# Performance work log

Hardware: AMD Instinct MI355X
Metric: run time of the kernel (lower is better)

Reference implementation:

```python
import jax, jax.numpy as jnp
import numpy as np

LN_EPS = 1e-5

def setup_inputs() -> dict:
    key = jax.random.key(0)
    ks = jax.random.split(key, 16)
    B, N, D, H = 8, 256, 128, 128
    s = 0.02
    inp = {
        'h': jax.random.normal(ks[0], (B, N, D), jnp.float32),
        'x': jax.random.normal(ks[1], (B, N, 3), jnp.float32),
        'mask': jax.random.randint(ks[2], (B, N), 0, 2, jnp.int32),
        # edge_mlp: Linear(2D+1,H), SiLU, Linear(H,H), SiLU
        'we1': jax.random.normal(ks[3], (2 * D + 1, H), jnp.float32) * s,
        'be1': jnp.zeros((H,), jnp.float32),
        'we2': jax.random.normal(ks[4], (H, H), jnp.float32) * s,
        'be2': jnp.zeros((H,), jnp.float32),
        # node_mlp: Linear(H+D,H), SiLU, Linear(H,D)
        'wn1': jax.random.normal(ks[5], (H + D, H), jnp.float32) * s,
        'bn1': jnp.zeros((H,), jnp.float32),
        'wn2': jax.random.normal(ks[6], (H, D), jnp.float32) * s,
        'bn2': jnp.zeros((D,), jnp.float32),
        # coord_mlp: Linear(H,H), SiLU, Linear(H,1,bias=False) xavier gain 1e-3, Tanh
        'wc1': jax.random.normal(ks[7], (H, H), jnp.float32) * s,
        'bc1': jnp.zeros((H,), jnp.float32),
        'wc2': jax.random.normal(ks[8], (H, 1), jnp.float32) * 0.001,
        # layer norm over output_nf
        'gamma': jnp.ones((D,), jnp.float32),
        'beta': jnp.zeros((D,), jnp.float32),
    }
    return inp


def reference(h, x, mask, we1, be1, we2, be2, wn1, bn1, wn2, bn2, wc1, bc1, wc2, gamma, beta):
    B, N, D = h.shape
    m = mask.astype(h.dtype)                      # [B,N]
    cm = m[:, :, None] * m[:, None, :]            # [B,N,N]

    hi = jnp.broadcast_to(h[:, :, None, :], (B, N, N, D))
    hj = jnp.broadcast_to(h[:, None, :, :], (B, N, N, D))
    rel_x = x[:, :, None, :] - x[:, None, :, :]   # [B,N,N,3]
    dist_sq = jnp.sum(rel_x * rel_x, axis=-1, keepdims=True) + 1e-8

    edge_input = jnp.concatenate([hi, hj, dist_sq], axis=-1)  # [B,N,N,2D+1]
    m_ij = jax.nn.silu(jax.nn.silu(edge_input @ we1 + be1) @ we2 + be2)
    m_ij = m_ij * cm[..., None]                   # [B,N,N,H]

    w_ij = jnp.tanh(jax.nn.silu(m_ij @ wc1 + bc1) @ wc2) * 0.1
    w_ij = w_ij * cm[..., None]                   # [B,N,N,1]

    coord_diff = jnp.sum(rel_x * w_ij, axis=2) / N
    x_out = x + coord_diff

    agg_m = jnp.sum(m_ij, axis=2)                 # [B,N,H]
    h_new = jax.nn.silu(jnp.concatenate([h, agg_m], axis=-1) @ wn1 + bn1) @ wn2 + bn2
    h2 = h + h_new

    mu = jnp.mean(h2, axis=-1, keepdims=True)
    var = jnp.mean((h2 - mu) ** 2, axis=-1, keepdims=True)
    h_out = (h2 - mu) * jax.lax.rsqrt(var + LN_EPS) * gamma + beta
    return (h_out, x_out)
```

## Files before the change

### kernel.cpp

```cpp
#include <hip/hip_runtime.h>
#include <hip/hip_bf16.h>

using short8 = __attribute__((ext_vector_type(8))) short;
using f32x4  = __attribute__((ext_vector_type(4))) float;

#define HD 128
#define NN 256
#define NB 2048

static __device__ __forceinline__ unsigned short us(float v) {
    union { __hip_bfloat16 b; unsigned short s; } c; c.b = __float2bfloat16(v); return c.s;
}
static __device__ __forceinline__ unsigned int pk2(float a, float b) {
    return (unsigned int)us(a) | ((unsigned int)us(b) << 16);
}
static __device__ __forceinline__ float fsilu(float v) {
    return __fdividef(v, 1.f + __expf(-v));
}
static __device__ __forceinline__ float ftanh(float v) {
    return 1.f - __fdividef(2.f, __expf(2.f * v) + 1.f);
}
static __device__ __forceinline__ int swz(int row, int kbyte) { return row * 256 + (kbyte ^ ((row & 7) << 4)); }
static __device__ __forceinline__ int swz512(int row, int kbyte) { return row * 512 + (kbyte ^ ((row & 7) << 4)); }

__global__ __launch_bounds__(256) void prep_all(
    const float* __restrict__ we2, const float* __restrict__ wc1,
    const float* __restrict__ wn1, const float* __restrict__ wn2,
    const float* __restrict__ we1, const int* __restrict__ mask,
    unsigned short* __restrict__ we2pk, unsigned short* __restrict__ wc1pk,
    unsigned short* __restrict__ wn1pk, unsigned short* __restrict__ wn2pk,
    unsigned short* __restrict__ we1pk,
    int* __restrict__ idxB, int* __restrict__ cntB)
{
    const int blk = blockIdx.x;
    const int t = threadIdx.x;
    if (blk < 448) {
        const int idx = blk * 256 + t;
        if (idx < 81920) {
            const float* src; unsigned short* dst; int local;
            if (idx < 16384)      { src = we2; dst = we2pk; local = idx;         }
            else if (idx < 32768) { src = wc1; dst = wc1pk; local = idx - 16384; }
            else if (idx < 65536) { src = wn1; dst = wn1pk; local = idx - 32768; }
            else                  { src = wn2; dst = wn2pk; local = idx - 65536; }
            const int k = local >> 7, n = local & 127;
            dst[((k >> 3) * 128 + n) * 8 + (k & 7)] = us(src[local]);
        } else {
            const int local = idx - 81920;
            const int k = local >> 8, n = local & 255;
            const int srci = (n < HD) ? (k * HD + n) : ((HD + k) * HD + (n - HD));
            we1pk[((k >> 3) * 256 + n) * 8 + (k & 7)] = us(we1[srci]);
        }
    } else {
        const int b = blk - 448;
        const int lane = t & 63, wvp = t >> 6;
        const int m = mask[b * NN + t];
        const unsigned long long bal = __ballot(m != 0);
        const int pos = __popcll(bal & ((1ULL << lane) - 1ULL));
        __shared__ int wc[4];
        if (lane == 0) wc[wvp] = __popcll(bal);
        __syncthreads();
        int base = 0;
        for (int w = 0; w < wvp; ++w) base += wc[w];
        const int cnt = wc[0] + wc[1] + wc[2] + wc[3];
        const int act_before = base + pos;
        const int slot = m ? act_before : cnt + (t - act_before);
        idxB[b * NN + slot] = t;
        if (t == 0) cntB[b] = cnt;
    }
}

__global__ __launch_bounds__(256) void prep_node_mfma(
    const float* __restrict__ h, const unsigned short* __restrict__ we1pk,
    const float* __restrict__ be1,
    float* __restrict__ Apre, float* __restrict__ Bpre)
{
    const int r0 = blockIdx.x * 16;
    const int tid = threadIdx.x;
    const int wv = tid >> 6, lane = tid & 63, g = lane >> 4, cl = lane & 15;
    __shared__ __align__(16) unsigned short t1[16 * HD];
    {
        const int row = tid >> 4, k0 = (tid & 15) * 8;
        const float4 a0 = *(const float4*)(h + (size_t)(r0 + row) * HD + k0);
        const float4 a1 = *(const float4*)(h + (size_t)(r0 + row) * HD + k0 + 4);
        uint4 o;
        o.x = pk2(a0.x, a0.y); o.y = pk2(a0.z, a0.w);
        o.z = pk2(a1.x, a1.y); o.w = pk2(a1.z, a1.w);
        *(uint4*)((char*)t1 + swz(row, 2 * k0)) = o;
    }
    __syncthreads();
    const f32x4 zero4 = {0.f, 0.f, 0.f, 0.f};
    f32x4 acc[4] = {zero4, zero4, zero4, zero4};
    #pragma unroll
    for (int ks = 0; ks < 4; ++ks) {
        const short8 a = *(const short8*)((char*)t1 + swz(cl, ks * 64 + g * 16));
        #pragma unroll
        for (int nt = 0; nt < 4; ++nt) {
            const int col = wv * 64 + nt * 16 + cl;
            const short8 bb = *(const short8*)(we1pk + ((ks * 4 + g) * 256 + col) * 8);
            acc[nt] = __builtin_amdgcn_mfma_f32_16x16x32_bf16(a, bb, acc[nt], 0, 0, 0);
        }
    }
    #pragma unroll
    for (int nt = 0; nt < 4; ++nt) {
        const int col = wv * 64 + nt * 16 + cl;
        const float bias = (col < HD) ? be1[col] : 0.f;
        #pragma unroll
        for (int r = 0; r < 4; ++r) {
            const int row = r0 + g * 4 + r;
            const float v = acc[nt][r] + bias;
            if (col < HD) Apre[(size_t)row * HD + col] = v;
            else          Bpre[(size_t)row * HD + (col - HD)] = v;
        }
    }
}

__global__ __launch_bounds__(256, 3) void egcl_main(
    const float* __restrict__ x, const float* __restrict__ we1,
    const float* __restrict__ be2, const float* __restrict__ bc1,
    const float* __restrict__ wc2,
    const float* __restrict__ Apre, const float* __restrict__ Bpre,
    const unsigned short* __restrict__ we2pk, const unsigned short* __restrict__ wc1pk,
    const int* __restrict__ idxB, const int* __restrict__ cntB,
    float* __restrict__ aggp, float4* __restrict__ cdws)
{
    const int blk = blockIdx.x;
    const int b = blk >> 9;
    const int q = blk & 511;
    const int p = q >> 1, hh = q & 1;
    const int tid = threadIdx.x;
    const int wv = tid >> 6, lane = tid & 63, g = lane >> 4, cl = lane & 15;

    const int cnt = cntB[b];
    const int i = idxB[b * NN + p];
    const int rowb = b * NN + i;

    const int nch_t = (cnt + 15) >> 4;
    const int c0 = ((nch_t + 1) >> 1) << 4;
    const int jbase = hh ? c0 : 0;
    const int jend  = hh ? cnt : (c0 < cnt ? c0 : cnt);
    const int hcnt  = jend - jbase;

    if (p >= cnt || hcnt <= 0) {
        if (tid < HD) aggp[((size_t)hh * NB + rowb) * HD + tid] = 0.f;
        if (tid == 0) cdws[hh * NB + rowb] = make_float4(0.f, 0.f, 0.f, 0.f);
        return;
    }

    __shared__ __align__(16) unsigned short m1[16 * HD];
    __shared__ __align__(16) unsigned short t2[16 * HD];
    __shared__ __align__(16) float4 jx_s[128];
    __shared__ int j_s[128];
    __shared__ __align__(16) float Ai_s[HD], wl_s[HD];
    __shared__ float sws[4][16];
    __shared__ float cdp[4][3];

    const float xi0 = x[rowb * 3 + 0];
    const float xi1 = x[rowb * 3 + 1];
    const float xi2 = x[rowb * 3 + 2];
    const int nch = (hcnt + 15) >> 4;

    if (tid < nch * 16) {
        const int j = (tid < hcnt) ? idxB[b * NN + jbase + tid] : i;
        const float* xj = x + (b * NN + j) * 3;
        const float x0 = xj[0], x1 = xj[1], x2 = xj[2];
        const float dx = xi0 - x0, dy = xi1 - x1, dz = xi2 - x2;
        float4 v; v.x = dx * dx + dy * dy + dz * dz + 1e-8f;
        v.y = x0; v.z = x1; v.w = x2;
        jx_s[tid] = v; j_s[tid] = j;
    }
    if (tid < HD) Ai_s[tid] = Apre[(size_t)rowb * HD + tid];
    else if (tid < 2 * HD) wl_s[tid - HD] = we1[2 * HD * HD + (tid - HD)];

    short8 bw2[4][2], bwc[4][2];
    #pragma unroll
    for (int ks = 0; ks < 4; ++ks) {
        #pragma unroll
        for (int nt = 0; nt < 2; ++nt) {
            const int off = ((ks * 4 + g) * HD + wv * 32 + nt * 16 + cl) * 8;
            bw2[ks][nt] = *(const short8*)(we2pk + off);
            bwc[ks][nt] = *(const short8*)(wc1pk + off);
        }
    }
    float be2v[2], bc1v[2], wc2v[2];
    #pragma unroll
    for (int nt = 0; nt < 2; ++nt) {
        const int col = wv * 32 + nt * 16 + cl;
        be2v[nt] = be2[col]; bc1v[nt] = bc1[col]; wc2v[nt] = wc2[col];
    }

    float agg[2] = {0.f, 0.f};
    float cdx = 0.f, cdy = 0.f, cdz = 0.f;
    const f32x4 zero4 = {0.f, 0.f, 0.f, 0.f};

    const int arow = tid >> 4;
    const int ak0  = (tid & 15) * 8;
    float4 sb0, sb1;

    #define ISSUE(C) do { \
        const float* bp_ = Bpre + (size_t)(b * NN + j_s[(C) * 16 + arow]) * HD + ak0; \
        sb0 = *(const float4*)(bp_); \
        sb1 = *(const float4*)(bp_ + 4); \
    } while (0)

    #define APHASE(C) do { \
        const float d2_ = jx_s[(C) * 16 + arow].x; \
        const float4 a0 = *(const float4*)(Ai_s + ak0); \
        const float4 a1 = *(const float4*)(Ai_s + ak0 + 4); \
        const float4 w0 = *(const float4*)(wl_s + ak0); \
        const float4 w1 = *(const float4*)(wl_s + ak0 + 4); \
        uint4 o; \
        o.x = pk2(fsilu(a0.x + sb0.x + d2_ * w0.x), fsilu(a0.y + sb0.y + d2_ * w0.y)); \
        o.y = pk2(fsilu(a0.z + sb0.z + d2_ * w0.z), fsilu(a0.w + sb0.w + d2_ * w0.w)); \
        o.z = pk2(fsilu(a1.x + sb1.x + d2_ * w1.x), fsilu(a1.y + sb1.y + d2_ * w1.y)); \
        o.w = pk2(fsilu(a1.z + sb1.z + d2_ * w1.z), fsilu(a1.w + sb1.w + d2_ * w1.w)); \
        *(uint4*)((char*)m1 + swz(arow, 2 * ak0)) = o; \
    } while (0)

    __syncthreads();
    ISSUE(0);
    APHASE(0);
    __syncthreads();

    for (int c = 0; c < nch; ++c) {
        f32x4 acc[2] = {zero4, zero4};
        #pragma unroll
        for (int ks = 0; ks < 4; ++ks) {
            const short8 a = *(const short8*)((char*)m1 + swz(cl, 2 * (ks * 32 + g * 8)));
            acc[0] = __builtin_amdgcn_mfma_f32_16x16x32_bf16(a, bw2[ks][0], acc[0], 0, 0, 0);
            acc[1] = __builtin_amdgcn_mfma_f32_16x16x32_bf16(a, bw2[ks][1], acc[1], 0, 0, 0);
        }
        #pragma unroll
        for (int nt = 0; nt < 2; ++nt) {
            const int col = wv * 32 + nt * 16 + cl;
            #pragma unroll
            for (int r = 0; r < 4; ++r) {
                const int row = g * 4 + r;
                const float mp = (c * 16 + row < hcnt) ? 1.f : 0.f;
                const float v = fsilu(acc[nt][r] + be2v[nt]) * mp;
                agg[nt] += v;
                *(unsigned short*)((char*)t2 + swz(row, 2 * col)) = us(v);
            }
        }
        __syncthreads();
        if (c + 1 < nch) ISSUE(c + 1);
        f32x4 acc2[2] = {zero4, zero4};
        #pragma unroll
        for (int ks = 0; ks < 4; ++ks) {
            const short8 a2 = *(const short8*)((char*)t2 + swz(cl, 2 * (ks * 32 + g * 8)));
            acc2[0] = __builtin_amdgcn_mfma_f32_16x16x32_bf16(a2, bwc[ks][0], acc2[0], 0, 0, 0);
            acc2[1] = __builtin_amdgcn_mfma_f32_16x16x32_bf16(a2, bwc[ks][1], acc2[1], 0, 0, 0);
        }
        #pragma unroll
        for (int r = 0; r < 4; ++r) {
            float sr = fsilu(acc2[0][r] + bc1v[0]) * wc2v[0]
                     + fsilu(acc2[1][r] + bc1v[1]) * wc2v[1];
            sr += __shfl_xor(sr, 1); sr += __shfl_xor(sr, 2);
            sr += __shfl_xor(sr, 4); sr += __shfl_xor(sr, 8);
            if (cl == 0) sws[wv][g * 4 + r] = sr;
        }
        if (c + 1 < nch) APHASE(c + 1);
        __syncthreads();
        if (tid < 16 && c * 16 + tid < hcnt) {
            const float s = sws[0][tid] + sws[1][tid] + sws[2][tid] + sws[3][tid];
            const float w = ftanh(s) * 0.1f;
            const float4 jx = jx_s[c * 16 + tid];
            cdx += (xi0 - jx.y) * w;
            cdy += (xi1 - jx.z) * w;
            cdz += (xi2 - jx.w) * w;
        }
    }
    #undef ISSUE
    #undef APHASE

    #pragma unroll
    for (int nt = 0; nt < 2; ++nt) {
        agg[nt] += __shfl_xor(agg[nt], 16);
        agg[nt] += __shfl_xor(agg[nt], 32);
    }
    if (lane < 16) {
        aggp[((size_t)hh * NB + rowb) * HD + wv * 32 + lane]      = agg[0];
        aggp[((size_t)hh * NB + rowb) * HD + wv * 32 + 16 + lane] = agg[1];
    }
    if (tid < 16) {
        cdx += __shfl_xor(cdx, 1); cdx += __shfl_xor(cdx, 2);
        cdx += __shfl_xor(cdx, 4); cdx += __shfl_xor(cdx, 8);
        cdy += __shfl_xor(cdy, 1); cdy += __shfl_xor(cdy, 2);
        cdy += __shfl_xor(cdy, 4); cdy += __shfl_xor(cdy, 8);
        cdz += __shfl_xor(cdz, 1); cdz += __shfl_xor(cdz, 2);
        cdz += __shfl_xor(cdz, 4); cdz += __shfl_xor(cdz, 8);
        if (tid == 0) {
            cdws[hh * NB + rowb] = make_float4(cdx, cdy, cdz, 0.f);
        }
    }
}

__global__ __launch_bounds__(256) void node_mlp(
    const float* __restrict__ h, const float* __restrict__ x,
    const float* __restrict__ aggp, const float4* __restrict__ cdws,
    const unsigned short* __restrict__ wn1pk, const unsigned short* __restrict__ wn2pk,
    const float* __restrict__ bn1, const float* __restrict__ bn2,
    const float* __restrict__ gamma, const float* __restrict__ beta,
    float* __restrict__ hout, float* __restrict__ xout)
{
    const int r0 = blockIdx.x * 16;
    const int tid = threadIdx.x;
    const int wv = tid >> 6, lane = tid & 63, g = lane >> 4, cl = lane & 15;
    __shared__ __align__(16) unsigned short t1[16 * 256];
    __shared__ __align__(16) unsigned short t2[16 * HD];
    __shared__ float rs1[4][16], rs2[4][16];
    __shared__ float bn1_s[HD], bn2_s[HD], gam_s[HD], bet_s[HD];
    if (tid < HD) {
        bn1_s[tid] = bn1[tid]; bn2_s[tid] = bn2[tid];
        gam_s[tid] = gamma[tid]; bet_s[tid] = beta[tid];
    }
    if (tid >= 128 && tid < 144) {
        const int row = r0 + (tid - 128);
        const float4 c0 = cdws[row], c1 = cdws[NB + row];
        xout[row * 3 + 0] = x[row * 3 + 0] + (c0.x + c1.x) * (1.f / 256.f);
        xout[row * 3 + 1] = x[row * 3 + 1] + (c0.y + c1.y) * (1.f / 256.f);
        xout[row * 3 + 2] = x[row * 3 + 2] + (c0.z + c1.z) * (1.f / 256.f);
    }
    {
        const int row = tid >> 4, k0 = (tid & 15) * 16;
        const size_t off = (size_t)(r0 + row) * HD;
        char* dst = (char*)t1;
        if (k0 < HD) {
            #pragma unroll
            for (int u = 0; u < 16; u += 8) {
                const float4 a0 = *(const float4*)(h + off + k0 + u);
                const float4 a1 = *(const float4*)(h + off + k0 + u + 4);
                uint4 o;
                o.x = pk2(a0.x, a0.y); o.y = pk2(a0.z, a0.w);
                o.z = pk2(a1.x, a1.y); o.w = pk2(a1.z, a1.w);
                *(uint4*)(dst + swz512(row, 2 * (k0 + u))) = o;
            }
        } else {
            const int kk = k0 - HD;
            #pragma unroll
            for (int u = 0; u < 16; u += 8) {
                const float4 a0 = *(const float4*)(aggp + off + kk + u);
                const float4 a1 = *(const float4*)(aggp + off + kk + u + 4);
                const float4 b0 = *(const float4*)(aggp + (size_t)NB * HD + off + kk + u);
                const float4 b1 = *(const float4*)(aggp + (size_t)NB * HD + off + kk + u + 4);
                uint4 o;
                o.x = pk2(a0.x + b0.x, a0.y + b0.y); o.y = pk2(a0.z + b0.z, a0.w + b0.w);
                o.z = pk2(a1.x + b1.x, a1.y + b1.y); o.w = pk2(a1.z + b1.z, a1.w + b1.w);
                *(uint4*)(dst + swz512(row, 2 * (k0 + u))) = o;
            }
        }
    }
    __syncthreads();
    const f32x4 zero4 = {0.f, 0.f, 0.f, 0.f};
    f32x4 acc[2] = {zero4, zero4};
    #pragma unroll
    for (int ks = 0; ks < 8; ++ks) {
        const short8 a = *(const short8*)((char*)t1 + swz512(cl, ks * 64 + g * 16));
        #pragma unroll
        for (int nt = 0; nt < 2; ++nt) {
            const int col = wv * 32 + nt * 16 + cl;
            const short8 bb = *(const short8*)(wn1pk + ((ks * 4 + g) * HD + col) * 8);
            acc[nt] = __builtin_amdgcn_mfma_f32_16x16x32_bf16(a, bb, acc[nt], 0, 0, 0);
        }
    }
    #pragma unroll
    for (int nt = 0; nt < 2; ++nt) {
        const int col = wv * 32 + nt * 16 + cl;
        const float bias = bn1_s[col];
        #pragma unroll
        for (int r = 0; r < 4; ++r) {
            const int row = g * 4 + r;
            *(unsigned short*)((char*)t2 + swz(row, 2 * col)) = us(fsilu(acc[nt][r] + bias));
        }
    }
    __syncthreads();
    f32x4 acc2[2] = {zero4, zero4};
    #pragma unroll
    for (int ks = 0; ks < 4; ++ks) {
        const short8 a = *(const short8*)((char*)t2 + swz(cl, ks * 64 + g * 16));
        #pragma unroll
        for (int nt = 0; nt < 2; ++nt) {
            const int col = wv * 32 + nt * 16 + cl;
            const short8 bb = *(const short8*)(wn2pk + ((ks * 4 + g) * HD + col) * 8);
            acc2[nt] = __builtin_amdgcn_mfma_f32_16x16x32_bf16(a, bb, acc2[nt], 0, 0, 0);
        }
    }
    float h2[2][4];
    #pragma unroll
    for (int nt = 0; nt < 2; ++nt) {
        const int col = wv * 32 + nt * 16 + cl;
        #pragma unroll
        for (int r = 0; r < 4; ++r) {
            const int row = g * 4 + r;
            h2[nt][r] = acc2[nt][r] + bn2_s[col] + h[(size_t)(r0 + row) * HD + col];
        }
    }
    #pragma unroll
    for (int r = 0; r < 4; ++r) {
        float pp = h2[0][r] + h2[1][r];
        pp += __shfl_xor(pp, 1); pp += __shfl_xor(pp, 2);
        pp += __shfl_xor(pp, 4); pp += __shfl_xor(pp, 8);
        if (cl == 0) rs1[wv][g * 4 + r] = pp;
    }
    __syncthreads();
    float mean[4];
    #pragma unroll
    for (int r = 0; r < 4; ++r) {
        const int row = g * 4 + r;
        mean[r] = (rs1[0][row] + rs1[1][row] + rs1[2][row] + rs1[3][row]) * (1.f / HD);
    }
    #pragma unroll
    for (int r = 0; r < 4; ++r) {
        const float d0 = h2[0][r] - mean[r], d1 = h2[1][r] - mean[r];
        float q = d0 * d0 + d1 * d1;
        q += __shfl_xor(q, 1); q += __shfl_xor(q, 2);
        q += __shfl_xor(q, 4); q += __shfl_xor(q, 8);
        if (cl == 0) rs2[wv][g * 4 + r] = q;
    }
    __syncthreads();
    #pragma unroll
    for (int r = 0; r < 4; ++r) {
        const int row = g * 4 + r;
        const float var = (rs2[0][row] + rs2[1][row] + rs2[2][row] + rs2[3][row]) * (1.f / HD);
        const float rsq = rsqrtf(var + 1e-5f);
        #pragma unroll
        for (int nt = 0; nt < 2; ++nt) {
            const int col = wv * 32 + nt * 16 + cl;
            hout[(size_t)(r0 + row) * HD + col] = (h2[nt][r] - mean[r]) * rsq * gam_s[col] + bet_s[col];
        }
    }
}

extern "C" void kernel_launch(void* const* d_in, const int* in_sizes, int n_in,
                              void* d_out, int out_size, void* d_ws, size_t ws_size,
                              hipStream_t stream)
{
    (void)in_sizes; (void)n_in; (void)out_size; (void)ws_size;
    const float* h     = (const float*)d_in[0];
    const float* x     = (const float*)d_in[1];
    const int*   mask  = (const int*)d_in[2];
    const float* we1   = (const float*)d_in[3];
    const float* be1   = (const float*)d_in[4];
    const float* we2   = (const float*)d_in[5];
    const float* be2   = (const float*)d_in[6];
    const float* wn1   = (const float*)d_in[7];
    const float* bn1   = (const float*)d_in[8];
    const float* wn2   = (const float*)d_in[9];
    const float* bn2   = (const float*)d_in[10];
    const float* wc1   = (const float*)d_in[11];
    const float* bc1   = (const float*)d_in[12];
    const float* wc2   = (const float*)d_in[13];
    const float* gamma = (const float*)d_in[14];
    const float* beta  = (const float*)d_in[15];

    float* out  = (float*)d_out;
    float* hout = out;
    float* xout = out + NB * HD;

    float* Apre  = (float*)d_ws;
    float* Bpre  = Apre + NB * HD;
    float* aggp  = Bpre + NB * HD;
    float4* cdws = (float4*)(aggp + 2 * NB * HD);
    unsigned short* we1pk = (unsigned short*)aggp;
    unsigned short* we2pk = (unsigned short*)(cdws + 2 * NB);
    unsigned short* wc1pk = we2pk + 128 * 128;
    unsigned short* wn1pk = wc1pk + 128 * 128;
    unsigned short* wn2pk = wn1pk + 256 * 128;
    int* idxB = (int*)(wn2pk + 128 * 128);
    int* cntB = idxB + 8 * NN;

    prep_all<<<456, 256, 0, stream>>>(we2, wc1, wn1, wn2, we1, mask,
                                      we2pk, wc1pk, wn1pk, wn2pk, we1pk, idxB, cntB);
    prep_node_mfma<<<128, 256, 0, stream>>>(h, we1pk, be1, Apre, Bpre);
    egcl_main<<<NB * 2, 256, 0, stream>>>(x, we1, be2, bc1, wc2,
                                          Apre, Bpre, we2pk, wc1pk, idxB, cntB,
                                          aggp, cdws);
    node_mlp<<<128, 256, 0, stream>>>(h, x, aggp, cdws, wn1pk, wn2pk,
                                      bn1, bn2, gamma, beta, hout, xout);
}
```

Measured before the change: 70.90 us.

## Double-buffer edge tiles and defer coordinate reduction to cut per-chunk barriers

Measured after the change: 71.02 us. No clear change (+0.2%).

```diff
diff --git a/kernel.cpp b/kernel.cpp
--- a/kernel.cpp
+++ b/kernel.cpp
@@ -146,12 +146,12 @@
         return;
     }
 
-    __shared__ __align__(16) unsigned short m1[16 * HD];
-    __shared__ __align__(16) unsigned short t2[16 * HD];
+    __shared__ __align__(16) unsigned short m1[2][16 * HD];
+    __shared__ __align__(16) unsigned short t2[2][16 * HD];
     __shared__ __align__(16) float4 jx_s[128];
     __shared__ int j_s[128];
     __shared__ __align__(16) float Ai_s[HD], wl_s[HD];
-    __shared__ float sws[4][16];
+    __shared__ float swsbuf[8][4][16];
     __shared__ float cdp[4][3];
 
     const float xi0 = x[rowb * 3 + 0];
@@ -189,7 +189,6 @@
     }
 
     float agg[2] = {0.f, 0.f};
-    float cdx = 0.f, cdy = 0.f, cdz = 0.f;
     const f32x4 zero4 = {0.f, 0.f, 0.f, 0.f};
 
     const int arow = tid >> 4;
@@ -213,7 +212,7 @@
         o.y = pk2(fsilu(a0.z + sb0.z + d2_ * w0.z), fsilu(a0.w + sb0.w + d2_ * w0.w)); \
         o.z = pk2(fsilu(a1.x + sb1.x + d2_ * w1.x), fsilu(a1.y + sb1.y + d2_ * w1.y)); \
         o.w = pk2(fsilu(a1.z + sb1.z + d2_ * w1.z), fsilu(a1.w + sb1.w + d2_ * w1.w)); \
-        *(uint4*)((char*)m1 + swz(arow, 2 * ak0)) = o; \
+        *(uint4*)((char*)m1[(C) & 1] + swz(arow, 2 * ak0)) = o; \
     } while (0)
 
     __syncthreads();
@@ -222,10 +221,13 @@
     __syncthreads();
 
     for (int c = 0; c < nch; ++c) {
+        const unsigned short* m1c = m1[c & 1];
+        unsigned short* t2c = t2[c & 1];
+        if (c + 1 < nch) ISSUE(c + 1);
         f32x4 acc[2] = {zero4, zero4};
         #pragma unroll
         for (int ks = 0; ks < 4; ++ks) {
-            const short8 a = *(const short8*)((char*)m1 + swz(cl, 2 * (ks * 32 + g * 8)));
+            const short8 a = *(const short8*)((const char*)m1c + swz(cl, 2 * (ks * 32 + g * 8)));
             acc[0] = __builtin_amdgcn_mfma_f32_16x16x32_bf16(a, bw2[ks][0], acc[0], 0, 0, 0);
             acc[1] = __builtin_amdgcn_mfma_f32_16x16x32_bf16(a, bw2[ks][1], acc[1], 0, 0, 0);
         }
@@ -238,15 +240,15 @@
                 const float mp = (c * 16 + row < hcnt) ? 1.f : 0.f;
                 const float v = fsilu(acc[nt][r] + be2v[nt]) * mp;
                 agg[nt] += v;
-                *(unsigned short*)((char*)t2 + swz(row, 2 * col)) = us(v);
+                *(unsigned short*)((char*)t2c + swz(row, 2 * col)) = us(v);
             }
         }
+        if (c + 1 < nch) APHASE(c + 1);
         __syncthreads();
-        if (c + 1 < nch) ISSUE(c + 1);
         f32x4 acc2[2] = {zero4, zero4};
         #pragma unroll
         for (int ks = 0; ks < 4; ++ks) {
-            const short8 a2 = *(const short8*)((char*)t2 + swz(cl, 2 * (ks * 32 + g * 8)));
+            const short8 a2 = *(const short8*)((const char*)t2c + swz(cl, 2 * (ks * 32 + g * 8)));
             acc2[0] = __builtin_amdgcn_mfma_f32_16x16x32_bf16(a2, bwc[ks][0], acc2[0], 0, 0, 0);
             acc2[1] = __builtin_amdgcn_mfma_f32_16x16x32_bf16(a2, bwc[ks][1], acc2[1], 0, 0, 0);
         }
@@ -256,21 +258,31 @@
                      + fsilu(acc2[1][r] + bc1v[1]) * wc2v[1];
             sr += __shfl_xor(sr, 1); sr += __shfl_xor(sr, 2);
             sr += __shfl_xor(sr, 4); sr += __shfl_xor(sr, 8);
-            if (cl == 0) sws[wv][g * 4 + r] = sr;
-        }
-        if (c + 1 < nch) APHASE(c + 1);
-        __syncthreads();
-        if (tid < 16 && c * 16 + tid < hcnt) {
-            const float s = sws[0][tid] + sws[1][tid] + sws[2][tid] + sws[3][tid];
-            const float w = ftanh(s) * 0.1f;
-            const float4 jx = jx_s[c * 16 + tid];
-            cdx += (xi0 - jx.y) * w;
-            cdy += (xi1 - jx.z) * w;
-            cdz += (xi2 - jx.w) * w;
+            if (cl == 0) swsbuf[c][wv][g * 4 + r] = sr;
         }
     }
     #undef ISSUE
     #undef APHASE
+    __syncthreads();
+
+    float cdx = 0.f, cdy = 0.f, cdz = 0.f;
+    if (tid < hcnt) {
+        const int ch = tid >> 4, row = tid & 15;
+        const float s = swsbuf[ch][0][row] + swsbuf[ch][1][row]
+                      + swsbuf[ch][2][row] + swsbuf[ch][3][row];
+        const float w = ftanh(s) * 0.1f;
+        const float4 jx = jx_s[tid];
+        cdx = (xi0 - jx.y) * w;
+        cdy = (xi1 - jx.z) * w;
+        cdz = (xi2 - jx.w) * w;
+    }
+    #pragma unroll
+    for (int m = 1; m <= 32; m <<= 1) {
+        cdx += __shfl_xor(cdx, m);
+        cdy += __shfl_xor(cdy, m);
+        cdz += __shfl_xor(cdz, m);
+    }
+    if (lane == 0) { cdp[wv][0] = cdx; cdp[wv][1] = cdy; cdp[wv][2] = cdz; }
 
     #pragma unroll
     for (int nt = 0; nt < 2; ++nt) {
@@ -281,16 +293,11 @@
         aggp[((size_t)hh * NB + rowb) * HD + wv * 32 + lane]      = agg[0];
         aggp[((size_t)hh * NB + rowb) * HD + wv * 32 + 16 + lane] = agg[1];
     }
-    if (tid < 16) {
-        cdx += __shfl_xor(cdx, 1); cdx += __shfl_xor(cdx, 2);
-        cdx += __shfl_xor(cdx, 4); cdx += __shfl_xor(cdx, 8);
-        cdy += __shfl_xor(cdy, 1); cdy += __shfl_xor(cdy, 2);
-        cdy += __shfl_xor(cdy, 4); cdy += __shfl_xor(cdy, 8);
-        cdz += __shfl_xor(cdz, 1); cdz += __shfl_xor(cdz, 2);
-        cdz += __shfl_xor(cdz, 4); cdz += __shfl_xor(cdz, 8);
-        if (tid == 0) {
-            cdws[hh * NB + rowb] = make_float4(cdx, cdy, cdz, 0.f);
-        }
+    __syncthreads();
+    if (tid == 0) {
+        cdws[hh * NB + rowb] = make_float4(cdp[0][0] + cdp[1][0] + cdp[2][0] + cdp[3][0],
+                                           cdp[0][1] + cdp[1][1] + cdp[2][1] + cdp[3][1],
+                                           cdp[0][2] + cdp[1][2] + cdp[2][2] + cdp[3][2], 0.f);
     }
 }
 
@@ -411,10 +418,10 @@
     #pragma unroll
     for (int r = 0; r < 4; ++r) {
         const float d0 = h2[0][r] - mean[r], d1 = h2[1][r] - mean[r];
-        float q = d0 * d0 + d1 * d1;
-        q += __shfl_xor(q, 1); q += __shfl_xor(q, 2);
-        q += __shfl_xor(q, 4); q += __shfl_xor(q, 8);
-        if (cl == 0) rs2[wv][g * 4 + r] = q;
+        float qq = d0 * d0 + d1 * d1;
+        qq += __shfl_xor(qq, 1); qq += __shfl_xor(qq, 2);
+        qq += __shfl_xor(qq, 4); qq += __shfl_xor(qq, 8);
+        if (cl == 0) rs2[wv][g * 4 + r] = qq;
     }
     __syncthreads();
     #pragma unroll
```
